# Optimization experiments

Measured on AMD Instinct MI355X. Metric: run time of the kernel, lower is better.

The kernel has to match this reference:

```python
import jax, jax.numpy as jnp
import numpy as np

N, D, H = 96, 64, 256  # num_nodes, input_dim, hidden_dim


def setup_inputs() -> dict:
    key = jax.random.key(0)
    ks = jax.random.split(key, 12)

    def lin(k, fan_in, fan_out):
        return jax.random.normal(k, (fan_in, fan_out), jnp.float32) / np.sqrt(fan_in)

    return {
        "node_features": jax.random.normal(ks[0], (N, D), jnp.float32),
        "edge_index": jax.random.randint(ks[1], (2, 1536), 0, N),
        # causal_discovery MLP: Linear(2D,H) -> ReLU -> Linear(H,H//2) -> ReLU -> Linear(H//2,1) -> Sigmoid
        "W1": lin(ks[2], 2 * D, H),      "b1": jnp.zeros((H,), jnp.float32),
        "W2": lin(ks[3], H, H // 2),     "b2": jnp.zeros((H // 2,), jnp.float32),
        "W3": lin(ks[4], H // 2, 1),     "b3": jnp.zeros((1,), jnp.float32),
        # confounder_detector MLP: Linear(3D,H) -> ReLU -> Linear(H,1) -> Sigmoid
        "V1": lin(ks[5], 3 * D, H),      "c1": jnp.zeros((H,), jnp.float32),
        "V2": lin(ks[6], H, 1),          "c2": jnp.zeros((1,), jnp.float32),
    }


def reference(node_features, edge_index, W1, b1, W2, b2, W3, b3, V1, c1, V2, c2):
    n, d = node_features.shape
    eye = jnp.eye(n, dtype=bool)

    # ---- discover_causal_structure: all ordered pairs (i, j), i != j ----
    # Linear on concat([x_i, x_j]) == x_i @ W1[:d] + x_j @ W1[d:] + b1
    pi = node_features @ W1[:d]           # [N, H]
    pj = node_features @ W1[d:]           # [N, H]
    h = jax.nn.relu(pi[:, None, :] + pj[None, :, :] + b1)   # [N, N, H]
    h = jax.nn.relu(h @ W2 + b2)                             # [N, N, H//2]
    causal = jax.nn.sigmoid((h @ W3 + b3)[..., 0])           # [N, N]
    causal = jnp.where(eye, 0.0, causal)                     # diagonal stays zero

    # ---- detect_confounders: all distinct triplets (i, j, k) ----
    ta = node_features @ V1[:d]            # [N, H]
    tb = node_features @ V1[d:2 * d]       # [N, H]
    tc = node_features @ V1[2 * d:]        # [N, H]
    t = jax.nn.relu(ta[:, None, None, :] + tb[None, :, None, :]
                    + tc[None, None, :, :] + c1)             # [N, N, N, H]
    conf = jax.nn.sigmoid((t @ V2 + c2)[..., 0])             # [N, N, N]
    distinct = (~eye[:, :, None]) & (~eye[None, :, :]) & (~eye[:, None, :])
    conf = jnp.where(distinct, conf, 0.0)

    return causal, conf
```

## Files before the change

### kernel.cpp

```cpp
#include <hip/hip_runtime.h>
#include <hip/hip_bf16.h>

#define NN 96
#define DD 64
#define HH 256
#define H2 128

typedef float v2f __attribute__((ext_vector_type(2)));

__global__ __launch_bounds__(256) void proj_kernel(
    const float* __restrict__ X, const float* __restrict__ W1, const float* __restrict__ b1,
    const float* __restrict__ V1, const float* __restrict__ c1,
    float* __restrict__ pi, float* __restrict__ pj,
    float* __restrict__ ta, float* __restrict__ tb, float* __restrict__ tcP)
{
    const int i = blockIdx.x;
    const int h = threadIdx.x;
    __shared__ float xs[DD];
    if (h < DD) xs[h] = X[i*DD + h];
    __syncthreads();
    float aPi = 0.f, aPj = 0.f, aTa = 0.f, aTb = 0.f, aTc = 0.f;
    #pragma unroll 8
    for (int d = 0; d < DD; ++d) {
        const float x = xs[d];
        aPi = fmaf(x, W1[d*HH + h],          aPi);
        aPj = fmaf(x, W1[(DD + d)*HH + h],   aPj);
        aTa = fmaf(x, V1[d*HH + h],          aTa);
        aTb = fmaf(x, V1[(DD + d)*HH + h],   aTb);
        aTc = fmaf(x, V1[(2*DD + d)*HH + h], aTc);
    }
    pi[i*HH + h] = aPi + b1[h];
    pj[i*HH + h] = aPj;
    ta[i*HH + h] = aTa + c1[h];
    tb[i*HH + h] = aTb;
    tcP[((h >> 1)*NN + i)*2 + (h & 1)] = aTc;
}

__global__ __launch_bounds__(256) void fused_kernel(
    const float* __restrict__ pi, const float* __restrict__ pj,
    const float* __restrict__ W2, const float* __restrict__ b2,
    const float* __restrict__ W3, const float* __restrict__ b3,
    const float* __restrict__ ta, const float* __restrict__ tb,
    const float* __restrict__ tcP, const float* __restrict__ V2,
    const float* __restrict__ c2, float* __restrict__ out)
{
    __shared__ float smem[4*64*2*12 + 2*12];
    const int i  = blockIdx.x;
    const int by = blockIdx.y;
    const int t  = threadIdx.x;

    if (by < 8) {
        const int j0 = by * 12;
        const int c2c = t & 63;
        const int qt  = t >> 6;

        float (*hb)[12]          = (float(*)[12])smem;
        float (*part)[64][2][12] = (float(*)[64][2][12])smem;
        float (*red)[12]         = (float(*)[12])(smem + 6144);

        {
            const float p_i = pi[i*HH + t];
            #pragma unroll
            for (int jj = 0; jj < 12; ++jj)
                hb[t][jj] = fmaxf(p_i + pj[(j0 + jj)*HH + t], 0.f);
        }
        __syncthreads();

        v2f acc0[6], acc1[6];
        #pragma unroll
        for (int p = 0; p < 6; ++p) { acc0[p] = (v2f)(0.f); acc1[p] = (v2f)(0.f); }

        const float* __restrict__ w2p = W2 + (qt*64)*H2 + c2c;
        #pragma unroll 2
        for (int q = 0; q < 64; ++q) {
            const float wa = w2p[q*H2];
            const float wb = w2p[q*H2 + 64];
            const v2f wa2 = {wa, wa};
            const v2f wb2 = {wb, wb};
            const int hq = qt*64 + q;
            const float4 hA = *(const float4*)&hb[hq][0];
            const float4 hB = *(const float4*)&hb[hq][4];
            const float4 hC = *(const float4*)&hb[hq][8];
            const v2f hp[6] = {{hA.x,hA.y},{hA.z,hA.w},
                               {hB.x,hB.y},{hB.z,hB.w},
                               {hC.x,hC.y},{hC.z,hC.w}};
            #pragma unroll
            for (int p = 0; p < 6; ++p) {
                acc0[p] += hp[p] * wa2;
                acc1[p] += hp[p] * wb2;
            }
        }
        __syncthreads();

        #pragma unroll
        for (int b = 0; b < 3; ++b) {
            float4 p0, p1;
            p0.x = acc0[b*2].x; p0.y = acc0[b*2].y; p0.z = acc0[b*2+1].x; p0.w = acc0[b*2+1].y;
            p1.x = acc1[b*2].x; p1.y = acc1[b*2].y; p1.z = acc1[b*2+1].x; p1.w = acc1[b*2+1].y;
            *(float4*)&part[qt][c2c][0][b*4] = p0;
            *(float4*)&part[qt][c2c][1][b*4] = p1;
        }
        __syncthreads();

        if (t < 128) {
            const int c  = t;
            const int cl = t & 63;
            const int cc = t >> 6;
            const float b2c = b2[c];
            const float w3c = W3[c];
            float v[12];
            #pragma unroll
            for (int b = 0; b < 3; ++b) {
                float4 s; s.x = 0.f; s.y = 0.f; s.z = 0.f; s.w = 0.f;
                #pragma unroll
                for (int qq = 0; qq < 4; ++qq) {
                    const float4 p = *(const float4*)&part[qq][cl][cc][b*4];
                    s.x += p.x; s.y += p.y; s.z += p.z; s.w += p.w;
                }
                v[b*4+0] = fmaxf(s.x + b2c, 0.f) * w3c;
                v[b*4+1] = fmaxf(s.y + b2c, 0.f) * w3c;
                v[b*4+2] = fmaxf(s.z + b2c, 0.f) * w3c;
                v[b*4+3] = fmaxf(s.w + b2c, 0.f) * w3c;
            }
            #pragma unroll
            for (int jj = 0; jj < 12; ++jj) {
                float s = v[jj];
                #pragma unroll
                for (int off = 32; off; off >>= 1) s += __shfl_down(s, off, 64);
                if ((t & 63) == 0) red[t >> 6][jj] = s;
            }
        }
        __syncthreads();
        if (t < 12) {
            const int j = j0 + t;
            const float s = red[0][t] + red[1][t] + b3[0];
            out[i*NN + j] = (i == j) ? 0.f : 1.f / (1.f + __expf(-s));
        }
    } else {
        const int j0 = (by - 8) * 12;
        float (*sbuf)[HH] = (float(*)[HH])smem;
        float* outc = out + NN*NN;

        for (int idx = t; idx < 12*HH/4; idx += 256) {
            const int jj = idx >> 6;
            const int h4 = (idx & 63) << 2;
            const float4 a = *(const float4*)&ta[i*HH + h4];
            const float4 b = *(const float4*)&tb[(j0 + jj)*HH + h4];
            float4 s; s.x = a.x + b.x; s.y = a.y + b.y; s.z = a.z + b.z; s.w = a.w + b.w;
            *(float4*)&sbuf[jj][h4] = s;
        }
        __syncthreads();

        if (t < 192) {
            const int g  = t / 48;
            const int l  = t % 48;
            const int k0 = 2*l;

            v2f acc[3][2];
            #pragma unroll
            for (int m = 0; m < 3; ++m) { acc[m][0] = (v2f)(0.f); acc[m][1] = (v2f)(0.f); }

            const float* __restrict__ sb0 = &sbuf[g*3 + 0][0];
            const float* __restrict__ sb1 = &sbuf[g*3 + 1][0];
            const float* __restrict__ sb2 = &sbuf[g*3 + 2][0];

            #pragma unroll 2
            for (int h0 = 0; h0 < HH; h0 += 4) {
                const float4 tA = *(const float4*)&tcP[((h0 >> 1)    *NN + k0)*2];
                const float4 tB = *(const float4*)&tcP[(((h0 >> 1)+1)*NN + k0)*2];
                const float4 vv = *(const float4*)&V2[h0];
                const float4 sA = *(const float4*)&sb0[h0];
                const float4 sB = *(const float4*)&sb1[h0];
                const float4 sC = *(const float4*)&sb2[h0];
                const v2f va01 = {vv.x, vv.y}, va23 = {vv.z, vv.w};
                const v2f tk0a = {tA.x, tA.y}, tk1a = {tA.z, tA.w};
                const v2f tk0b = {tB.x, tB.y}, tk1b = {tB.z, tB.w};
                const v2f sp[3][2] = {{{sA.x,sA.y},{sA.z,sA.w}},
                                      {{sB.x,sB.y},{sB.z,sB.w}},
                                      {{sC.x,sC.y},{sC.z,sC.w}}};
                #pragma unroll
                for (int m = 0; m < 3; ++m) {
                    v2f x;
                    x = sp[m][0] + tk0a;
                    x.x = fmaxf(x.x, 0.f); x.y = fmaxf(x.y, 0.f);
                    acc[m][0] += x * va01;
                    x = sp[m][0] + tk1a;
                    x.x = fmaxf(x.x, 0.f); x.y = fmaxf(x.y, 0.f);
                    acc[m][1] += x * va01;
                    x = sp[m][1] + tk0b;
                    x.x = fmaxf(x.x, 0.f); x.y = fmaxf(x.y, 0.f);
                    acc[m][0] += x * va23;
                    x = sp[m][1] + tk1b;
                    x.x = fmaxf(x.x, 0.f); x.y = fmaxf(x.y, 0.f);
                    acc[m][1] += x * va23;
                }
            }

            const float c2v = c2[0];
            #pragma unroll
            for (int m = 0; m < 3; ++m) {
                const int j = j0 + g*3 + m;
                const float a0 = acc[m][0].x + acc[m][0].y;
                const float a1 = acc[m][1].x + acc[m][1].y;
                float2 o;
                o.x = 1.f / (1.f + __expf(-(a0 + c2v)));
                o.y = 1.f / (1.f + __expf(-(a1 + c2v)));
                if (i == j || i == k0   || j == k0  ) o.x = 0.f;
                if (i == j || i == k0+1 || j == k0+1) o.y = 0.f;
                *(float2*)&outc[(i*NN + j)*NN + k0] = o;
            }
        }
    }
}

extern "C" void kernel_launch(void* const* d_in, const int* in_sizes, int n_in,
                              void* d_out, int out_size, void* d_ws, size_t ws_size,
                              hipStream_t stream) {
    const float* X  = (const float*)d_in[0];
    const float* W1 = (const float*)d_in[2];
    const float* b1 = (const float*)d_in[3];
    const float* W2 = (const float*)d_in[4];
    const float* b2 = (const float*)d_in[5];
    const float* W3 = (const float*)d_in[6];
    const float* b3 = (const float*)d_in[7];
    const float* V1 = (const float*)d_in[8];
    const float* c1 = (const float*)d_in[9];
    const float* V2 = (const float*)d_in[10];
    const float* c2 = (const float*)d_in[11];

    float* out = (float*)d_out;
    float* ws  = (float*)d_ws;
    float* pi  = ws;
    float* pj  = pi + NN*HH;
    float* ta  = pj + NN*HH;
    float* tb  = ta + NN*HH;
    float* tcP = tb + NN*HH;

    proj_kernel<<<NN, 256, 0, stream>>>(X, W1, b1, V1, c1, pi, pj, ta, tb, tcP);
    fused_kernel<<<dim3(NN, 16), 256, 0, stream>>>(pi, pj, W2, b2, W3, b3,
                                                   ta, tb, tcP, V2, c2, out);
}
```

Baseline: 40.88 us.

## Halve shared memory via two-stage partial reduction and shrink confounder tiles

The causal branch now reduces its four K-quarter partials in two stages (the upper half adds into the lower half), which halves the shared buffer so more blocks fit per CU. Launch bounds request 8 blocks per SM. The confounder branch handles 6 j values per block instead of 12, with each thread owning one j and 3 k values, and the grid grows from 16 to 24 y-blocks. This trades an extra barrier and smaller per-thread register reuse of tcP loads for higher occupancy and more blocks.

```diff
diff --git a/kernel.cpp b/kernel.cpp
--- a/kernel.cpp
+++ b/kernel.cpp
@@ -36,7 +36,7 @@
     tcP[((h >> 1)*NN + i)*2 + (h & 1)] = aTc;
 }
 
-__global__ __launch_bounds__(256) void fused_kernel(
+__global__ __launch_bounds__(256, 8) void fused_kernel(
     const float* __restrict__ pi, const float* __restrict__ pj,
     const float* __restrict__ W2, const float* __restrict__ b2,
     const float* __restrict__ W3, const float* __restrict__ b3,
@@ -44,7 +44,7 @@
     const float* __restrict__ tcP, const float* __restrict__ V2,
     const float* __restrict__ c2, float* __restrict__ out)
 {
-    __shared__ float smem[4*64*2*12 + 2*12];
+    __shared__ float smem[3072 + 24];
     const int i  = blockIdx.x;
     const int by = blockIdx.y;
     const int t  = threadIdx.x;
@@ -56,7 +56,7 @@
 
         float (*hb)[12]          = (float(*)[12])smem;
         float (*part)[64][2][12] = (float(*)[64][2][12])smem;
-        float (*red)[12]         = (float(*)[12])(smem + 6144);
+        float (*red)[12]         = (float(*)[12])(smem + 3072);
 
         {
             const float p_i = pi[i*HH + t];
@@ -92,35 +92,44 @@
         }
         __syncthreads();
 
-        #pragma unroll
-        for (int b = 0; b < 3; ++b) {
-            float4 p0, p1;
-            p0.x = acc0[b*2].x; p0.y = acc0[b*2].y; p0.z = acc0[b*2+1].x; p0.w = acc0[b*2+1].y;
-            p1.x = acc1[b*2].x; p1.y = acc1[b*2].y; p1.z = acc1[b*2+1].x; p1.w = acc1[b*2+1].y;
-            *(float4*)&part[qt][c2c][0][b*4] = p0;
-            *(float4*)&part[qt][c2c][1][b*4] = p1;
+        if (qt < 2) {
+            #pragma unroll
+            for (int b = 0; b < 3; ++b) {
+                float4 p0, p1;
+                p0.x = acc0[b*2].x; p0.y = acc0[b*2].y; p0.z = acc0[b*2+1].x; p0.w = acc0[b*2+1].y;
+                p1.x = acc1[b*2].x; p1.y = acc1[b*2].y; p1.z = acc1[b*2+1].x; p1.w = acc1[b*2+1].y;
+                *(float4*)&part[qt][c2c][0][b*4] = p0;
+                *(float4*)&part[qt][c2c][1][b*4] = p1;
+            }
+        }
+        __syncthreads();
+        if (qt >= 2) {
+            #pragma unroll
+            for (int b = 0; b < 3; ++b) {
+                float4 p0 = *(const float4*)&part[qt-2][c2c][0][b*4];
+                float4 p1 = *(const float4*)&part[qt-2][c2c][1][b*4];
+                p0.x += acc0[b*2].x; p0.y += acc0[b*2].y; p0.z += acc0[b*2+1].x; p0.w += acc0[b*2+1].y;
+                p1.x += acc1[b*2].x; p1.y += acc1[b*2].y; p1.z += acc1[b*2+1].x; p1.w += acc1[b*2+1].y;
+                *(float4*)&part[qt-2][c2c][0][b*4] = p0;
+                *(float4*)&part[qt-2][c2c][1][b*4] = p1;
+            }
         }
         __syncthreads();
 
         if (t < 128) {
-            const int c  = t;
             const int cl = t & 63;
             const int cc = t >> 6;
-            const float b2c = b2[c];
-            const float w3c = W3[c];
+            const float b2c = b2[t];
+            const float w3c = W3[t];
             float v[12];
             #pragma unroll
             for (int b = 0; b < 3; ++b) {
-                float4 s; s.x = 0.f; s.y = 0.f; s.z = 0.f; s.w = 0.f;
-                #pragma unroll
-                for (int qq = 0; qq < 4; ++qq) {
-                    const float4 p = *(const float4*)&part[qq][cl][cc][b*4];
-                    s.x += p.x; s.y += p.y; s.z += p.z; s.w += p.w;
-                }
-                v[b*4+0] = fmaxf(s.x + b2c, 0.f) * w3c;
-                v[b*4+1] = fmaxf(s.y + b2c, 0.f) * w3c;
-                v[b*4+2] = fmaxf(s.z + b2c, 0.f) * w3c;
-                v[b*4+3] = fmaxf(s.w + b2c, 0.f) * w3c;
+                const float4 pa = *(const float4*)&part[0][cl][cc][b*4];
+                const float4 pb = *(const float4*)&part[1][cl][cc][b*4];
+                v[b*4+0] = fmaxf(pa.x + pb.x + b2c, 0.f) * w3c;
+                v[b*4+1] = fmaxf(pa.y + pb.y + b2c, 0.f) * w3c;
+                v[b*4+2] = fmaxf(pa.z + pb.z + b2c, 0.f) * w3c;
+                v[b*4+3] = fmaxf(pa.w + pb.w + b2c, 0.f) * w3c;
             }
             #pragma unroll
             for (int jj = 0; jj < 12; ++jj) {
@@ -137,11 +146,11 @@
             out[i*NN + j] = (i == j) ? 0.f : 1.f / (1.f + __expf(-s));
         }
     } else {
-        const int j0 = (by - 8) * 12;
+        const int j0 = (by - 8) * 6;
         float (*sbuf)[HH] = (float(*)[HH])smem;
         float* outc = out + NN*NN;
 
-        for (int idx = t; idx < 12*HH/4; idx += 256) {
+        for (int idx = t; idx < 6*HH/4; idx += 256) {
             const int jj = idx >> 6;
             const int h4 = (idx & 63) << 2;
             const float4 a = *(const float4*)&ta[i*HH + h4];
@@ -152,62 +161,58 @@
         __syncthreads();
 
         if (t < 192) {
-            const int g  = t / 48;
-            const int l  = t % 48;
-            const int k0 = 2*l;
-
-            v2f acc[3][2];
-            #pragma unroll
-            for (int m = 0; m < 3; ++m) { acc[m][0] = (v2f)(0.f); acc[m][1] = (v2f)(0.f); }
-
-            const float* __restrict__ sb0 = &sbuf[g*3 + 0][0];
-            const float* __restrict__ sb1 = &sbuf[g*3 + 1][0];
-            const float* __restrict__ sb2 = &sbuf[g*3 + 2][0];
+            const int jg = t >> 5;
+            const int l  = t & 31;
+            const int k0 = 3*l;
+
+            v2f acc[3];
+            acc[0] = (v2f)(0.f); acc[1] = (v2f)(0.f); acc[2] = (v2f)(0.f);
+
+            const float* __restrict__ sb = &sbuf[jg][0];
 
             #pragma unroll 2
             for (int h0 = 0; h0 < HH; h0 += 4) {
-                const float4 tA = *(const float4*)&tcP[((h0 >> 1)    *NN + k0)*2];
-                const float4 tB = *(const float4*)&tcP[(((h0 >> 1)+1)*NN + k0)*2];
+                const int hp = h0 >> 1;
+                const float2 tA0 = *(const float2*)&tcP[(hp*NN + k0 + 0)*2];
+                const float2 tA1 = *(const float2*)&tcP[(hp*NN + k0 + 1)*2];
+                const float2 tA2 = *(const float2*)&tcP[(hp*NN + k0 + 2)*2];
+                const float2 tB0 = *(const float2*)&tcP[((hp+1)*NN + k0 + 0)*2];
+                const float2 tB1 = *(const float2*)&tcP[((hp+1)*NN + k0 + 1)*2];
+                const float2 tB2 = *(const float2*)&tcP[((hp+1)*NN + k0 + 2)*2];
                 const float4 vv = *(const float4*)&V2[h0];
-                const float4 sA = *(const float4*)&sb0[h0];
-                const float4 sB = *(const float4*)&sb1[h0];
-                const float4 sC = *(const float4*)&sb2[h0];
+                const float4 sA = *(const float4*)&sb[h0];
+                const v2f sp0 = {sA.x, sA.y}, sp1 = {sA.z, sA.w};
                 const v2f va01 = {vv.x, vv.y}, va23 = {vv.z, vv.w};
-                const v2f tk0a = {tA.x, tA.y}, tk1a = {tA.z, tA.w};
-                const v2f tk0b = {tB.x, tB.y}, tk1b = {tB.z, tB.w};
-                const v2f sp[3][2] = {{{sA.x,sA.y},{sA.z,sA.w}},
-                                      {{sB.x,sB.y},{sB.z,sB.w}},
-                                      {{sC.x,sC.y},{sC.z,sC.w}}};
-                #pragma unroll
-                for (int m = 0; m < 3; ++m) {
-                    v2f x;
-                    x = sp[m][0] + tk0a;
-                    x.x = fmaxf(x.x, 0.f); x.y = fmaxf(x.y, 0.f);
-                    acc[m][0] += x * va01;
-                    x = sp[m][0] + tk1a;
-                    x.x = fmaxf(x.x, 0.f); x.y = fmaxf(x.y, 0.f);
-                    acc[m][1] += x * va01;
-                    x = sp[m][1] + tk0b;
-                    x.x = fmaxf(x.x, 0.f); x.y = fmaxf(x.y, 0.f);
-                    acc[m][0] += x * va23;
-                    x = sp[m][1] + tk1b;
-                    x.x = fmaxf(x.x, 0.f); x.y = fmaxf(x.y, 0.f);
-                    acc[m][1] += x * va23;
-                }
+                v2f x;
+                x = sp0 + (v2f){tA0.x, tA0.y};
+                x.x = fmaxf(x.x, 0.f); x.y = fmaxf(x.y, 0.f);
+                acc[0] += x * va01;
+                x = sp1 + (v2f){tB0.x, tB0.y};
+                x.x = fmaxf(x.x, 0.f); x.y = fmaxf(x.y, 0.f);
+                acc[0] += x * va23;
+                x = sp0 + (v2f){tA1.x, tA1.y};
+                x.x = fmaxf(x.x, 0.f); x.y = fmaxf(x.y, 0.f);
+                acc[1] += x * va01;
+                x = sp1 + (v2f){tB1.x, tB1.y};
+                x.x = fmaxf(x.x, 0.f); x.y = fmaxf(x.y, 0.f);
+                acc[1] += x * va23;
+                x = sp0 + (v2f){tA2.x, tA2.y};
+                x.x = fmaxf(x.x, 0.f); x.y = fmaxf(x.y, 0.f);
+                acc[2] += x * va01;
+                x = sp1 + (v2f){tB2.x, tB2.y};
+                x.x = fmaxf(x.x, 0.f); x.y = fmaxf(x.y, 0.f);
+                acc[2] += x * va23;
             }
 
             const float c2v = c2[0];
-            #pragma unroll
-            for (int m = 0; m < 3; ++m) {
-                const int j = j0 + g*3 + m;
-                const float a0 = acc[m][0].x + acc[m][0].y;
-                const float a1 = acc[m][1].x + acc[m][1].y;
-                float2 o;
-                o.x = 1.f / (1.f + __expf(-(a0 + c2v)));
-                o.y = 1.f / (1.f + __expf(-(a1 + c2v)));
-                if (i == j || i == k0   || j == k0  ) o.x = 0.f;
-                if (i == j || i == k0+1 || j == k0+1) o.y = 0.f;
-                *(float2*)&outc[(i*NN + j)*NN + k0] = o;
+            const int j = j0 + jg;
+            #pragma unroll
+            for (int kk = 0; kk < 3; ++kk) {
+                const int k = k0 + kk;
+                const float a = acc[kk].x + acc[kk].y;
+                float val = 1.f / (1.f + __expf(-(a + c2v)));
+                if (i == j || i == k || j == k) val = 0.f;
+                outc[(i*NN + j)*NN + k] = val;
             }
         }
     }
@@ -237,6 +242,6 @@
     float* tcP = tb + NN*HH;
 
     proj_kernel<<<NN, 256, 0, stream>>>(X, W1, b1, V1, c1, pi, pj, ta, tb, tcP);
-    fused_kernel<<<dim3(NN, 16), 256, 0, stream>>>(pi, pj, W2, b2, W3, b3,
+    fused_kernel<<<dim3(NN, 24), 256, 0, stream>>>(pi, pj, W2, b2, W3, b3,
                                                    ta, tb, tcP, V2, c2, out);
 }
```

After: 51.21 us. 1.25x slower.
